# Kernel optimization log

Hardware: AMD Instinct MI355X
Metric: run time of the kernel (lower is better)

## Reference

```python
import jax, jax.numpy as jnp
import numpy as np

N = 100000   # nodes
E = 1600000  # edges (avg degree 16)
D = 128      # in_dim


def setup_inputs() -> dict:
    key = jax.random.key(0)
    k = jax.random.split(key, 8)
    h = jax.random.normal(k[0], (N, D), dtype=jnp.float32)
    d = jax.random.uniform(k[1], (N,), dtype=jnp.float32)  # per-node degree norm (e.g. deg^-0.5)
    yes_no = jax.random.uniform(k[2], (E,), dtype=jnp.float32)
    gate_w = jax.random.normal(k[3], (1, 2 * D), dtype=jnp.float32) * (1.414 / np.sqrt(2 * D))
    gate_b = jnp.zeros((1,), dtype=jnp.float32)
    yes_weight = jax.random.uniform(k[4], (), dtype=jnp.float32)
    no_weight = jax.random.uniform(k[5], (), dtype=jnp.float32)
    src = jax.random.randint(k[6], (E,), 0, N, dtype=jnp.int64)
    dst = jax.random.randint(k[7], (E,), 0, N, dtype=jnp.int64)
    return {"h": h, "d": d, "yes_no": yes_no, "gate_w": gate_w, "gate_b": gate_b,
            "yes_weight": yes_weight, "no_weight": no_weight, "src": src, "dst": dst}


def reference(h, d, yes_no, gate_w, gate_b, yes_weight, no_weight, src, dst):
    n, dim = h.shape
    # gate(cat[h_dst, h_src]) == h_dst @ W[:, :D].T + h_src @ W[:, D:].T + b
    # project once per node, then gather per edge (avoids [E, 2D] concat)
    p_dst = h @ gate_w[0, :dim]  # [N]
    p_src = h @ gate_w[0, dim:]  # [N]
    g = jnp.tanh(p_dst[dst] + p_src[src] + gate_b[0])  # [E]
    yn = jnp.tanh(yes_no * yes_weight + (1.0 - yes_no) * no_weight)  # [E]
    e = (g + yn) * 0.5 * d[dst] * d[src]  # [E] (dropout p=0 -> identity)
    m = h[src] * e[:, None]  # [E, D] edge messages
    z = jax.ops.segment_sum(m, dst, num_segments=n)  # [N, D]
    return z
```

## Files before the change

### kernel.cpp

```cpp
#include <hip/hip_runtime.h>

#define D 128
#define CAP 64

__device__ __forceinline__ unsigned short f2bf(float x) {
    unsigned int u = __float_as_uint(x);
    u += 0x7FFFu + ((u >> 16) & 1u);
    return (unsigned short)(u >> 16);
}
__device__ __forceinline__ float bf2f(unsigned short b) {
    return __uint_as_float(((unsigned int)b) << 16);
}

__global__ __launch_bounds__(256) void proj_kernel(const float* __restrict__ h,
                                                   const float* __restrict__ gw,
                                                   const float* __restrict__ dnorm,
                                                   float4* __restrict__ q,
                                                   unsigned short* __restrict__ hb,
                                                   int n_nodes) {
    int node = (int)((blockIdx.x * blockDim.x + threadIdx.x) >> 6);
    int lane = threadIdx.x & 63;
    if (node >= n_nodes) return;
    const float2* hr2 = (const float2*)(h + (size_t)node * D);
    const float2* gw2 = (const float2*)gw;
    float2 hv = hr2[lane];
    float2 wa = gw2[lane];
    float2 wb = gw2[lane + 64];
    ushort2 hvb = make_ushort2(f2bf(hv.x), f2bf(hv.y));
    *(ushort2*)(hb + (size_t)node * D + 2 * lane) = hvb;
    float s1 = hv.x * wa.x + hv.y * wa.y;
    float s2 = hv.x * wb.x + hv.y * wb.y;
    #pragma unroll
    for (int off = 32; off > 0; off >>= 1) {
        s1 += __shfl_down(s1, off, 64);
        s2 += __shfl_down(s2, off, 64);
    }
    if (lane == 0) q[node] = make_float4(s1, s2, dnorm[node], 0.0f);
}

__global__ __launch_bounds__(256) void fill_kernel(const float4* __restrict__ q,
                                                   const float* __restrict__ yes_no,
                                                   const int* __restrict__ src,
                                                   const int* __restrict__ dst,
                                                   const float* __restrict__ gate_b,
                                                   const float* __restrict__ yes_w,
                                                   const float* __restrict__ no_w,
                                                   int* __restrict__ cnt,
                                                   unsigned int* __restrict__ csr,
                                                   int n_edges) {
    int i = blockIdx.x * blockDim.x + threadIdx.x;
    int e0 = 2 * i;
    if (e0 >= n_edges) return;
    float gb = gate_b[0];
    float yw = yes_w[0];
    float nw = no_w[0];
    bool has1 = (e0 + 1) < n_edges;

    int2 sv, tv;
    float2 ynv;
    if (has1) {
        sv = *(const int2*)(src + e0);
        tv = *(const int2*)(dst + e0);
        ynv = *(const float2*)(yes_no + e0);
    } else {
        sv = make_int2(src[e0], 0);
        tv = make_int2(dst[e0], 0);
        ynv = make_float2(yes_no[e0], 0.0f);
    }

    float4 qt0 = q[tv.x];
    float4 qs0 = q[sv.x];
    float4 qt1, qs1;
    if (has1) { qt1 = q[tv.y]; qs1 = q[sv.y]; }

    {
        float g = tanhf(qt0.x + qs0.y + gb);
        float y = tanhf(ynv.x * yw + (1.0f - ynv.x) * nw);
        float ce = (g + y) * 0.5f * qt0.z * qs0.z;
        int qv = (int)rintf(ce * 8191.0f) + 8192;
        unsigned int entry = ((unsigned int)sv.x << 15) | (unsigned int)qv;
        int pos = atomicAdd(&cnt[tv.x], 1);
        if (pos < CAP)
            __builtin_nontemporal_store(entry, &csr[(size_t)tv.x * CAP + pos]);
    }
    if (has1) {
        float g = tanhf(qt1.x + qs1.y + gb);
        float y = tanhf(ynv.y * yw + (1.0f - ynv.y) * nw);
        float ce = (g + y) * 0.5f * qt1.z * qs1.z;
        int qv = (int)rintf(ce * 8191.0f) + 8192;
        unsigned int entry = ((unsigned int)sv.y << 15) | (unsigned int)qv;
        int pos = atomicAdd(&cnt[tv.y], 1);
        if (pos < CAP)
            __builtin_nontemporal_store(entry, &csr[(size_t)tv.y * CAP + pos]);
    }
}

__global__ __launch_bounds__(256) void gather_kernel(const unsigned short* __restrict__ hb,
                                                     const int* __restrict__ cnt,
                                                     const unsigned int* __restrict__ csr,
                                                     float4* __restrict__ z4,
                                                     int n_nodes) {
    int node = (int)((blockIdx.x * blockDim.x + threadIdx.x) >> 5);
    int lane = threadIdx.x & 31;
    if (node >= n_nodes) return;
    int n = cnt[node];
    if (n > CAP) n = CAP;
    const unsigned int* row = csr + (size_t)node * CAP;
    float4 acc = make_float4(0.0f, 0.0f, 0.0f, 0.0f);
    const float inv = 1.0f / 8191.0f;
    int k = 0;
    for (; k + 3 < n; k += 4) {
        unsigned int e0 = row[k], e1 = row[k + 1], e2 = row[k + 2], e3 = row[k + 3];
        float c0 = (float)((int)(e0 & 0x7fffu) - 8192) * inv;
        float c1 = (float)((int)(e1 & 0x7fffu) - 8192) * inv;
        float c2 = (float)((int)(e2 & 0x7fffu) - 8192) * inv;
        float c3 = (float)((int)(e3 & 0x7fffu) - 8192) * inv;
        ushort4 a = *(const ushort4*)(hb + (size_t)(e0 >> 15) * D + 4 * lane);
        ushort4 b = *(const ushort4*)(hb + (size_t)(e1 >> 15) * D + 4 * lane);
        ushort4 c = *(const ushort4*)(hb + (size_t)(e2 >> 15) * D + 4 * lane);
        ushort4 d = *(const ushort4*)(hb + (size_t)(e3 >> 15) * D + 4 * lane);
        acc.x += bf2f(a.x) * c0 + bf2f(b.x) * c1 + bf2f(c.x) * c2 + bf2f(d.x) * c3;
        acc.y += bf2f(a.y) * c0 + bf2f(b.y) * c1 + bf2f(c.y) * c2 + bf2f(d.y) * c3;
        acc.z += bf2f(a.z) * c0 + bf2f(b.z) * c1 + bf2f(c.z) * c2 + bf2f(d.z) * c3;
        acc.w += bf2f(a.w) * c0 + bf2f(b.w) * c1 + bf2f(c.w) * c2 + bf2f(d.w) * c3;
    }
    for (; k < n; ++k) {
        unsigned int e0 = row[k];
        float c0 = (float)((int)(e0 & 0x7fffu) - 8192) * inv;
        ushort4 a = *(const ushort4*)(hb + (size_t)(e0 >> 15) * D + 4 * lane);
        acc.x += bf2f(a.x) * c0;
        acc.y += bf2f(a.y) * c0;
        acc.z += bf2f(a.z) * c0;
        acc.w += bf2f(a.w) * c0;
    }
    z4[(size_t)node * (D / 4) + lane] = acc;
}

extern "C" void kernel_launch(void* const* d_in, const int* in_sizes, int n_in,
                              void* d_out, int out_size, void* d_ws, size_t ws_size,
                              hipStream_t stream) {
    const float* h       = (const float*)d_in[0];
    const float* dnorm   = (const float*)d_in[1];
    const float* yes_no  = (const float*)d_in[2];
    const float* gate_w  = (const float*)d_in[3];
    const float* gate_b  = (const float*)d_in[4];
    const float* yes_w   = (const float*)d_in[5];
    const float* no_w    = (const float*)d_in[6];
    const int*   src     = (const int*)d_in[7];
    const int*   dst     = (const int*)d_in[8];

    int n_nodes = in_sizes[0] / D;
    int n_edges = in_sizes[2];

    char* ws = (char*)d_ws;
    size_t off = 0;
    auto take = [&](size_t bytes) {
        void* ptr = ws + off;
        off += (bytes + 15) & ~(size_t)15;
        return ptr;
    };
    float4*         q   = (float4*)take((size_t)n_nodes * sizeof(float4));
    unsigned short* hb  = (unsigned short*)take((size_t)n_nodes * D * sizeof(unsigned short));
    int*            cnt = (int*)take((size_t)n_nodes * sizeof(int));
    unsigned int*   csr = (unsigned int*)take((size_t)n_nodes * CAP * sizeof(unsigned int));
    (void)ws_size;

    hipMemsetAsync(cnt, 0, (size_t)n_nodes * sizeof(int), stream);

    proj_kernel<<<(n_nodes + 3) / 4, 256, 0, stream>>>(h, gate_w, dnorm, q, hb, n_nodes);

    int nt = (n_edges + 1) / 2;
    fill_kernel<<<(nt + 255) / 256, 256, 0, stream>>>(
        q, yes_no, src, dst, gate_b, yes_w, no_w, cnt, csr, n_edges);

    gather_kernel<<<(n_nodes + 7) / 8, 256, 0, stream>>>(
        hb, cnt, csr, (float4*)d_out, n_nodes);
}
```

Before: 279.1 us.

## Split edge fill into record stream plus destination-partitioned scatter pass

Edge coefficient computation now writes packed (dst, entry) records sequentially, and a new scatter kernel performs the atomic slot allocation and CSR store. The scatter grid processes eight destination partitions, each block re-reading an edge stripe and handling only edges whose dst falls in its partition, so that atomics and stores touch a smaller working set. This trades extra record traffic (an intermediate buffer written once and read eight times) and an additional launch for more cache-local random atomics.

```diff
diff --git a/kernel.cpp b/kernel.cpp
--- a/kernel.cpp
+++ b/kernel.cpp
@@ -2,6 +2,8 @@
 
 #define D 128
 #define CAP 64
+
+typedef unsigned int uint4n __attribute__((ext_vector_type(4)));
 
 __device__ __forceinline__ unsigned short f2bf(float x) {
     unsigned int u = __float_as_uint(x);
@@ -38,16 +40,15 @@
     if (lane == 0) q[node] = make_float4(s1, s2, dnorm[node], 0.0f);
 }
 
-__global__ __launch_bounds__(256) void fill_kernel(const float4* __restrict__ q,
-                                                   const float* __restrict__ yes_no,
-                                                   const int* __restrict__ src,
-                                                   const int* __restrict__ dst,
-                                                   const float* __restrict__ gate_b,
-                                                   const float* __restrict__ yes_w,
-                                                   const float* __restrict__ no_w,
-                                                   int* __restrict__ cnt,
-                                                   unsigned int* __restrict__ csr,
-                                                   int n_edges) {
+__global__ __launch_bounds__(256) void stream_kernel(const float4* __restrict__ q,
+                                                     const float* __restrict__ yes_no,
+                                                     const int* __restrict__ src,
+                                                     const int* __restrict__ dst,
+                                                     const float* __restrict__ gate_b,
+                                                     const float* __restrict__ yes_w,
+                                                     const float* __restrict__ no_w,
+                                                     uint2* __restrict__ rec,
+                                                     int n_edges) {
     int i = blockIdx.x * blockDim.x + threadIdx.x;
     int e0 = 2 * i;
     if (e0 >= n_edges) return;
@@ -78,20 +79,48 @@
         float y = tanhf(ynv.x * yw + (1.0f - ynv.x) * nw);
         float ce = (g + y) * 0.5f * qt0.z * qs0.z;
         int qv = (int)rintf(ce * 8191.0f) + 8192;
-        unsigned int entry = ((unsigned int)sv.x << 15) | (unsigned int)qv;
-        int pos = atomicAdd(&cnt[tv.x], 1);
-        if (pos < CAP)
-            __builtin_nontemporal_store(entry, &csr[(size_t)tv.x * CAP + pos]);
+        rec[e0] = make_uint2((unsigned int)tv.x,
+                             ((unsigned int)sv.x << 15) | (unsigned int)qv);
     }
     if (has1) {
         float g = tanhf(qt1.x + qs1.y + gb);
         float y = tanhf(ynv.y * yw + (1.0f - ynv.y) * nw);
         float ce = (g + y) * 0.5f * qt1.z * qs1.z;
         int qv = (int)rintf(ce * 8191.0f) + 8192;
-        unsigned int entry = ((unsigned int)sv.y << 15) | (unsigned int)qv;
-        int pos = atomicAdd(&cnt[tv.y], 1);
-        if (pos < CAP)
-            __builtin_nontemporal_store(entry, &csr[(size_t)tv.y * CAP + pos]);
+        rec[e0 + 1] = make_uint2((unsigned int)tv.y,
+                                 ((unsigned int)sv.y << 15) | (unsigned int)qv);
+    }
+}
+
+__global__ __launch_bounds__(256) void scatter_kernel(const uint2* __restrict__ rec,
+                                                      int* __restrict__ cnt,
+                                                      unsigned int* __restrict__ csr,
+                                                      int n_edges,
+                                                      int psize,
+                                                      int ngroups) {
+    unsigned int p = blockIdx.x & 7;
+    int g = blockIdx.x >> 3;
+    int stripe = (n_edges + ngroups - 1) / ngroups;
+    int beg = g * stripe;
+    int end = min(n_edges, beg + stripe);
+    for (int i = beg + 2 * (int)threadIdx.x; i < end; i += 512) {
+        uint2 r0, r1;
+        bool two = (i + 1) < end;
+        if (two) {
+            uint4n rr = __builtin_nontemporal_load((const uint4n*)(rec + i));
+            r0 = make_uint2(rr.x, rr.y);
+            r1 = make_uint2(rr.z, rr.w);
+        } else {
+            r0 = rec[i];
+        }
+        if (r0.x / (unsigned int)psize == p) {
+            int pos = atomicAdd(&cnt[r0.x], 1);
+            if (pos < CAP) csr[(size_t)r0.x * CAP + pos] = r0.y;
+        }
+        if (two && (r1.x / (unsigned int)psize == p)) {
+            int pos = atomicAdd(&cnt[r1.x], 1);
+            if (pos < CAP) csr[(size_t)r1.x * CAP + pos] = r1.y;
+        }
     }
 }
 
@@ -151,6 +180,7 @@
 
     int n_nodes = in_sizes[0] / D;
     int n_edges = in_sizes[2];
+    int psize   = (n_nodes + 7) / 8;
 
     char* ws = (char*)d_ws;
     size_t off = 0;
@@ -162,16 +192,21 @@
     float4*         q   = (float4*)take((size_t)n_nodes * sizeof(float4));
     unsigned short* hb  = (unsigned short*)take((size_t)n_nodes * D * sizeof(unsigned short));
     int*            cnt = (int*)take((size_t)n_nodes * sizeof(int));
+    uint2*          rec = (uint2*)take((size_t)n_edges * sizeof(uint2));
     unsigned int*   csr = (unsigned int*)take((size_t)n_nodes * CAP * sizeof(unsigned int));
     (void)ws_size;
 
-    hipMemsetAsync(cnt, 0, (size_t)n_nodes * sizeof(int), stream);
+    (void)hipMemsetAsync(cnt, 0, (size_t)n_nodes * sizeof(int), stream);
 
     proj_kernel<<<(n_nodes + 3) / 4, 256, 0, stream>>>(h, gate_w, dnorm, q, hb, n_nodes);
 
     int nt = (n_edges + 1) / 2;
-    fill_kernel<<<(nt + 255) / 256, 256, 0, stream>>>(
-        q, yes_no, src, dst, gate_b, yes_w, no_w, cnt, csr, n_edges);
+    stream_kernel<<<(nt + 255) / 256, 256, 0, stream>>>(
+        q, yes_no, src, dst, gate_b, yes_w, no_w, rec, n_edges);
+
+    int ngroups = 256;
+    scatter_kernel<<<ngroups * 8, 256, 0, stream>>>(
+        rec, cnt, csr, n_edges, psize, ngroups);
 
     gather_kernel<<<(n_nodes + 7) / 8, 256, 0, stream>>>(
         hb, cnt, csr, (float4*)d_out, n_nodes);
```

Result: slower. 296.7 us (+6.3%).
